# Kernel tuning notes

Hardware: AMD Instinct MI355X
Metric: run time of the kernel (lower is better)

The kernel has to match this reference:

```python
import jax, jax.numpy as jnp
import numpy as np

LOOKBACK = 1
LOOKAHEAD = 0
SEQ, BATCH, IN, HID = 1024, 16, 1024, 1024
K = LOOKBACK + 1 + LOOKAHEAD


def quick_gelu(x):
    return x * jax.nn.sigmoid(1.702 * x)


def setup_inputs() -> dict:
    key = jax.random.key(0)
    ks = jax.random.split(key, 5)
    scale = 1.0 / np.sqrt(IN * K)  # like torch Conv1d default init scale
    X = jax.random.normal(ks[0], (SEQ, BATCH, IN), dtype=jnp.float32)
    Wz = jax.random.normal(ks[1], (HID, IN, K), dtype=jnp.float32) * scale
    bz = jax.random.normal(ks[2], (HID,), dtype=jnp.float32) * scale
    Wf = jax.random.normal(ks[3], (HID, IN, K), dtype=jnp.float32) * scale
    bf = jax.random.normal(ks[4], (HID,), dtype=jnp.float32) * scale
    return {"X": X, "Wz": Wz, "bz": bz, "Wf": Wf, "bf": bf}


def _conv1d(x_pad, W, b):
    # x_pad: (B, Cin, T+K-1), W: (Cout, Cin, K) -> (B, Cout, T)
    y = jax.lax.conv_general_dilated(
        x_pad, W, window_strides=(1,), padding="VALID",
        dimension_numbers=("NCH", "OIH", "NCH"))
    return y + b[None, :, None]


def reference(X, Wz, bz, Wf, bf):
    # pad time dim: lookback zeros before, lookahead zeros after
    X_pad = jnp.pad(X, ((LOOKBACK, LOOKAHEAD), (0, 0), (0, 0)))
    X_pad = jnp.transpose(X_pad, (1, 2, 0))  # (B, Cin, T+K-1)
    Z = jnp.transpose(_conv1d(X_pad, Wz, bz), (2, 0, 1))  # (T, B, H)
    F = jnp.transpose(_conv1d(X_pad, Wf, bf), (2, 0, 1))  # (T, B, H)
    Z = quick_gelu(Z)
    F = jax.nn.sigmoid(F)

    def step(h, fz):
        f, z = fz
        h = f * z + (1.0 - f) * h
        return h, h

    h0 = jnp.zeros((BATCH, HID), dtype=X.dtype)
    _, H = jax.lax.scan(step, h0, (F, Z))  # H: (T, B, HID)
    return H, H[-1:, :, :]
```

## Files before the change

### kernel.cpp

```cpp
#include <hip/hip_runtime.h>
#include <stdint.h>

#define T_SEQ 1024
#define B_SZ  16
#define C_IN  1024
#define C_HID 1024
#define M_ROWS (T_SEQ * B_SZ)
#define N_COLS (2 * C_HID)
#define K_DIM  (2 * C_IN)

#define NCHUNK 16
#define CLEN   (T_SEQ / NCHUNK)
#define NBH    (B_SZ * C_HID)

typedef __attribute__((ext_vector_type(8))) short bf16x8;
typedef __attribute__((ext_vector_type(4))) float f32x4;
typedef unsigned short u16;

__device__ __forceinline__ u16 f2bf(float f) {
  union { float f; unsigned u; } v; v.f = f;
  unsigned r = v.u + 0x7fffu + ((v.u >> 16) & 1u);
  return (u16)(r >> 16);
}
__device__ __forceinline__ float bf2f(unsigned s) {
  union { unsigned u; float f; } v; v.u = s << 16;
  return v.f;
}

__device__ __forceinline__ void async_cp16(const u16* g, u16* l) {
  __builtin_amdgcn_global_load_lds(
      (const __attribute__((address_space(1))) unsigned*)(uintptr_t)g,
      (__attribute__((address_space(3))) unsigned*)(uintptr_t)l,
      16, 0, 0);
}

__global__ void k_convert_x(const float* __restrict__ X, u16* __restrict__ Xp) {
  int i = blockIdx.x * 256 + threadIdx.x;
  const int total4 = (M_ROWS + B_SZ) * C_IN / 4;
  if (i >= total4) return;
  int e = i << 2;
  const int PAD = B_SZ * C_IN;
  ushort4 o;
  if (e < PAD) {
    o.x = o.y = o.z = o.w = 0;
  } else {
    float4 v = *reinterpret_cast<const float4*>(X + (e - PAD));
    o.x = f2bf(v.x); o.y = f2bf(v.y); o.z = f2bf(v.z); o.w = f2bf(v.w);
  }
  *reinterpret_cast<ushort4*>(Xp + e) = o;
}

__global__ void k_repack_w(const float* __restrict__ Wz, const float* __restrict__ Wf,
                           u16* __restrict__ Wt) {
  int i = blockIdx.x * 256 + threadIdx.x;
  if (i >= 2 * 1024 * 1024) return;
  int g  = i >> 20;
  int hc = i & ((1 << 20) - 1);
  int h  = hc >> 10;
  int c  = hc & 1023;
  const float* W = g ? Wf : Wz;
  float2 w = *reinterpret_cast<const float2*>(W + ((size_t)(h << 10) + c) * 2);
  size_t n = ((size_t)h << 1) | (size_t)g;
  Wt[n * K_DIM + c]        = f2bf(w.x);
  Wt[n * K_DIM + 1024 + c] = f2bf(w.y);
}

__global__ __launch_bounds__(256, 2) void k_gemm(const u16* __restrict__ Xp,
                                                 const u16* __restrict__ Wt,
                                                 const float* __restrict__ bz,
                                                 const float* __restrict__ bfv,
                                                 u16* __restrict__ Cb) {
  __shared__ u16 sA[128 * 64];
  __shared__ u16 sB[128 * 64];
  const int tid  = threadIdx.x;
  const int wid  = tid >> 6;
  const int lane = tid & 63;
  const int m0 = blockIdx.x << 7;
  const int n0 = blockIdx.y << 7;
  const int wr = wid >> 1, wc = wid & 1;

  f32x4 acc[4][4] = {};

  const int srow = (wid << 5) + (lane >> 3);
  const int scol = (lane & 7) << 3;
  const int lr = lane & 15;
  const int lk = (lane >> 4) << 3;

  u16* lA = &sA[(wid << 5) << 6];
  u16* lB = &sB[(wid << 5) << 6];

  for (int kt = 0; kt < 32; ++kt) {
    const u16* gA = Xp + (size_t)(m0 + ((kt >= 16) ? B_SZ : 0) + srow) * C_IN
                       + ((kt & 15) << 6) + scol;
    const u16* gB = Wt + (size_t)(n0 + srow) * K_DIM + (kt << 6) + scol;
#pragma unroll
    for (int i = 0; i < 4; ++i) {
      async_cp16(gA + (size_t)(i << 3) * C_IN, lA + ((i << 3) << 6));
      async_cp16(gB + (size_t)(i << 3) * K_DIM, lB + ((i << 3) << 6));
    }
    __syncthreads();

#pragma unroll
    for (int ks = 0; ks < 2; ++ks) {
      bf16x8 a[4], b[4];
#pragma unroll
      for (int mi = 0; mi < 4; ++mi)
        a[mi] = *reinterpret_cast<const bf16x8*>(
            &sA[(((wr << 6) + (mi << 4) + lr) << 6) + (ks << 5) + lk]);
#pragma unroll
      for (int ni = 0; ni < 4; ++ni)
        b[ni] = *reinterpret_cast<const bf16x8*>(
            &sB[(((wc << 6) + (ni << 4) + lr) << 6) + (ks << 5) + lk]);
#pragma unroll
      for (int mi = 0; mi < 4; ++mi)
#pragma unroll
        for (int ni = 0; ni < 4; ++ni)
          acc[mi][ni] = __builtin_amdgcn_mfma_f32_16x16x32_bf16(
              a[mi], b[ni], acc[mi][ni], 0, 0, 0);
    }
    __syncthreads();
  }

  const int erow = (lane >> 4) << 2;
  const int ecol = lane & 15;
#pragma unroll
  for (int ni = 0; ni < 4; ++ni) {
    int col  = n0 + (wc << 6) + (ni << 4) + ecol;
    int hcol = col >> 1;
    bool isz = (col & 1) == 0;
    float bias = isz ? bz[hcol] : bfv[hcol];
    float kk   = isz ? 1.702f : 1.0f;
#pragma unroll
    for (int mi = 0; mi < 4; ++mi) {
      int row = m0 + (wr << 6) + (mi << 4) + erow;
#pragma unroll
      for (int r = 0; r < 4; ++r) {
        float v = acc[mi][ni][r] + bias;
        float s = 1.f / (1.f + __expf(-kk * v));
        float res = isz ? v * s : s;
        Cb[(size_t)(row + r) * N_COLS + col] = f2bf(res);
      }
    }
  }
}

__global__ __launch_bounds__(256) void k_scan1(const u16* __restrict__ Cb,
                                               float* __restrict__ Ap,
                                               float* __restrict__ Bp) {
  int i = blockIdx.x * 256 + threadIdx.x;
  int h = i & (C_HID - 1);
  int b = (i >> 10) & (B_SZ - 1);
  int c = i >> 14;
  const unsigned* Cu = (const unsigned*)Cb;
  size_t base = (size_t)b * C_HID + h + (size_t)c * CLEN * NBH;
  float hh = 0.f, P = 1.f;
#pragma unroll 16
  for (int t = 0; t < CLEN; ++t) {
    unsigned zf = Cu[base + (size_t)t * NBH];
    float z = bf2f(zf & 0xffffu);
    float f = bf2f(zf >> 16);
    hh += f * (z - hh);
    P  *= (1.f - f);
  }
  Ap[i] = hh;
  Bp[i] = P;
}

__global__ __launch_bounds__(256) void k_scan2(const float* __restrict__ Ap,
                                               const float* __restrict__ Bp,
                                               float* __restrict__ St) {
  int i = blockIdx.x * 256 + threadIdx.x;
  float hh = 0.f;
#pragma unroll
  for (int c = 0; c < NCHUNK; ++c) {
    St[c * NBH + i] = hh;
    hh = Ap[c * NBH + i] + Bp[c * NBH + i] * hh;
  }
}

__global__ __launch_bounds__(256) void k_scan3(const u16* __restrict__ Cb,
                                               const float* __restrict__ St,
                                               float* __restrict__ out) {
  int i = blockIdx.x * 256 + threadIdx.x;
  int bh = i & (NBH - 1);
  int c = i >> 14;
  const unsigned* Cu = (const unsigned*)Cb;
  size_t base = (size_t)bh + (size_t)c * CLEN * NBH;
  float hh = St[i];
#pragma unroll 16
  for (int t = 0; t < CLEN; ++t) {
    unsigned zf = Cu[base + (size_t)t * NBH];
    float z = bf2f(zf & 0xffffu);
    float f = bf2f(zf >> 16);
    hh += f * (z - hh);
    out[base + (size_t)t * NBH] = hh;
  }
  if (c == NCHUNK - 1)
    out[(size_t)M_ROWS * C_HID + bh] = hh;
}

extern "C" void kernel_launch(void* const* d_in, const int* in_sizes, int n_in,
                              void* d_out, int out_size, void* d_ws, size_t ws_size,
                              hipStream_t stream) {
  const float* X   = (const float*)d_in[0];
  const float* Wz  = (const float*)d_in[1];
  const float* bz  = (const float*)d_in[2];
  const float* Wf  = (const float*)d_in[3];
  const float* bf_ = (const float*)d_in[4];
  float* out = (float*)d_out;

  u16* Xp = (u16*)d_ws;
  u16* Wt = Xp + (size_t)(M_ROWS + B_SZ) * C_IN;
  u16* Cb = Wt + (size_t)N_COLS * K_DIM;
  float* Ap = (float*)Xp;
  float* Bp = Ap + NCHUNK * NBH;
  float* St = Bp + NCHUNK * NBH;

  hipLaunchKernelGGL(k_convert_x, dim3(16400), dim3(256), 0, stream, X, Xp);
  hipLaunchKernelGGL(k_repack_w, dim3(8192), dim3(256), 0, stream, Wz, Wf, Wt);
  hipLaunchKernelGGL(k_gemm, dim3(M_ROWS / 128, N_COLS / 128), dim3(256), 0, stream,
                     Xp, Wt, bz, bf_, Cb);
  hipLaunchKernelGGL(k_scan1, dim3(NCHUNK * NBH / 256), dim3(256), 0, stream,
                     Cb, Ap, Bp);
  hipLaunchKernelGGL(k_scan2, dim3(NBH / 256), dim3(256), 0, stream, Ap, Bp, St);
  hipLaunchKernelGGL(k_scan3, dim3(NCHUNK * NBH / 256), dim3(256), 0, stream,
                     Cb, St, out);
}
```

Before: 328.7 us.

## Rewrite GEMM as 256x256 tile, 8-wave, double-buffered pipelined kernel with swizzled LDS

Replaces the 128x128 single-buffered GEMM with a 256x256-tile kernel using 8 waves and double-buffered LDS. Global-to-LDS async loads are issued in quarter stages interleaved with MFMA phases, paced by explicit vmcnt waits, barriers and setprio. An XOR swizzle on the LDS layout is meant to avoid bank conflicts, and block indices are remapped for better L2 locality. The aim is to hide load latency and raise MFMA utilisation, at the cost of higher register pressure (32 accumulators per lane) and fragile hand-written wait counts.

```diff
diff --git a/kernel.cpp b/kernel.cpp
--- a/kernel.cpp
+++ b/kernel.cpp
@@ -16,6 +16,8 @@
 typedef __attribute__((ext_vector_type(8))) short bf16x8;
 typedef __attribute__((ext_vector_type(4))) float f32x4;
 typedef unsigned short u16;
+
+#define MFMA __builtin_amdgcn_mfma_f32_16x16x32_bf16
 
 __device__ __forceinline__ u16 f2bf(float f) {
   union { float f; unsigned u; } v; v.f = f;
@@ -65,60 +67,142 @@
   Wt[n * K_DIM + 1024 + c] = f2bf(w.y);
 }
 
-__global__ __launch_bounds__(256, 2) void k_gemm(const u16* __restrict__ Xp,
-                                                 const u16* __restrict__ Wt,
-                                                 const float* __restrict__ bz,
-                                                 const float* __restrict__ bfv,
-                                                 u16* __restrict__ Cb) {
-  __shared__ u16 sA[128 * 64];
-  __shared__ u16 sB[128 * 64];
+__global__ __launch_bounds__(512, 2) void k_gemm8(const u16* __restrict__ Xp,
+                                                  const u16* __restrict__ Wt,
+                                                  const float* __restrict__ bz,
+                                                  const float* __restrict__ bfv,
+                                                  u16* __restrict__ Cb) {
+  __shared__ u16 lds[2][2][2][8192];
   const int tid  = threadIdx.x;
+  const int lane = tid & 63;
   const int wid  = tid >> 6;
-  const int lane = tid & 63;
-  const int m0 = blockIdx.x << 7;
-  const int n0 = blockIdx.y << 7;
-  const int wr = wid >> 1, wc = wid & 1;
-
-  f32x4 acc[4][4] = {};
-
-  const int srow = (wid << 5) + (lane >> 3);
-  const int scol = (lane & 7) << 3;
+  const int wr = wid >> 2;
+  const int wc = wid & 3;
   const int lr = lane & 15;
-  const int lk = (lane >> 4) << 3;
-
-  u16* lA = &sA[(wid << 5) << 6];
-  u16* lB = &sB[(wid << 5) << 6];
-
-  for (int kt = 0; kt < 32; ++kt) {
-    const u16* gA = Xp + (size_t)(m0 + ((kt >= 16) ? B_SZ : 0) + srow) * C_IN
-                       + ((kt & 15) << 6) + scol;
-    const u16* gB = Wt + (size_t)(n0 + srow) * K_DIM + (kt << 6) + scol;
-#pragma unroll
-    for (int i = 0; i < 4; ++i) {
-      async_cp16(gA + (size_t)(i << 3) * C_IN, lA + ((i << 3) << 6));
-      async_cp16(gB + (size_t)(i << 3) * K_DIM, lB + ((i << 3) << 6));
+
+  int wg = (blockIdx.x & 7) * 64 + (blockIdx.x >> 3);
+  const int m0 = (wg >> 3) << 8;
+  const int n0 = (wg & 7) << 8;
+
+  const int p    = tid << 4;
+  const int q    = p ^ (((p >> 7) & 7) << 4);
+  const int grow = q >> 7;
+  const int gcol = (q & 127) >> 1;
+  const int ldsw = (tid >> 6) << 9;
+
+  const int rbase = lr << 6;
+  int co[2];
+#pragma unroll
+  for (int ks = 0; ks < 2; ++ks)
+    co[ks] = ((((ks << 6) | ((lane >> 4) << 4)) ^ ((lr & 7) << 4)) >> 1);
+
+  auto stage = [&](int j) {
+    int kt = j >> 2, part = j & 3, buf = kt & 1;
+    if (part >= 2) {
+      int h = part - 2;
+      const u16* g = Xp + (size_t)(m0 + (h << 7) + grow + ((kt >= 16) ? B_SZ : 0)) * C_IN
+                        + ((kt & 15) << 6) + gcol;
+      u16* l = &lds[buf][0][h][ldsw];
+      async_cp16(g, l);
+      async_cp16(g + (size_t)64 * C_IN, l + 4096);
+    } else {
+      const u16* g = Wt + (size_t)(n0 + (part << 7) + grow) * K_DIM + (kt << 6) + gcol;
+      u16* l = &lds[buf][1][part][ldsw];
+      async_cp16(g, l);
+      async_cp16(g + (size_t)64 * K_DIM, l + 4096);
     }
-    __syncthreads();
-
-#pragma unroll
-    for (int ks = 0; ks < 2; ++ks) {
-      bf16x8 a[4], b[4];
-#pragma unroll
-      for (int mi = 0; mi < 4; ++mi)
-        a[mi] = *reinterpret_cast<const bf16x8*>(
-            &sA[(((wr << 6) + (mi << 4) + lr) << 6) + (ks << 5) + lk]);
-#pragma unroll
-      for (int ni = 0; ni < 4; ++ni)
-        b[ni] = *reinterpret_cast<const bf16x8*>(
-            &sB[(((wc << 6) + (ni << 4) + lr) << 6) + (ks << 5) + lk]);
-#pragma unroll
-      for (int mi = 0; mi < 4; ++mi)
-#pragma unroll
-        for (int ni = 0; ni < 4; ++ni)
-          acc[mi][ni] = __builtin_amdgcn_mfma_f32_16x16x32_bf16(
-              a[mi], b[ni], acc[mi][ni], 0, 0, 0);
-    }
-    __syncthreads();
+  };
+
+  f32x4 acc[8][4] = {};
+  bf16x8 a[4][2], b0[2][2], b1[2][2];
+
+  for (int j = 0; j < 7; ++j) stage(j);
+  asm volatile("s_waitcnt vmcnt(6)" ::: "memory");
+  __builtin_amdgcn_s_barrier();
+
+#pragma unroll 2
+  for (int t = 0; t < 32; ++t) {
+    const int buf = t & 1;
+    const u16* pA = &lds[buf][0][wr][0];
+    const u16* pB = &lds[buf][1][wc >> 1][(wc & 1) << 12];
+    const int jb = 4 * t + 7;
+
+#pragma unroll
+    for (int mi = 0; mi < 4; ++mi)
+#pragma unroll
+      for (int ks = 0; ks < 2; ++ks)
+        a[mi][ks] = *(const bf16x8*)(pA + (mi << 10) + rbase + co[ks]);
+#pragma unroll
+    for (int ni = 0; ni < 2; ++ni)
+#pragma unroll
+      for (int ks = 0; ks < 2; ++ks)
+        b0[ni][ks] = *(const bf16x8*)(pB + (ni << 10) + rbase + co[ks]);
+    if (jb < 128) stage(jb);
+    __builtin_amdgcn_s_barrier();
+    asm volatile("s_waitcnt lgkmcnt(0)" ::: "memory");
+    __builtin_amdgcn_s_setprio(1);
+#pragma unroll
+    for (int mi = 0; mi < 4; ++mi)
+#pragma unroll
+      for (int ni = 0; ni < 2; ++ni)
+#pragma unroll
+        for (int ks = 0; ks < 2; ++ks)
+          acc[mi][ni] = MFMA(a[mi][ks], b0[ni][ks], acc[mi][ni], 0, 0, 0);
+    __builtin_amdgcn_s_setprio(0);
+    __builtin_amdgcn_s_barrier();
+
+#pragma unroll
+    for (int ni = 0; ni < 2; ++ni)
+#pragma unroll
+      for (int ks = 0; ks < 2; ++ks)
+        b1[ni][ks] = *(const bf16x8*)(pB + ((2 + ni) << 10) + rbase + co[ks]);
+    if (jb + 1 < 128) stage(jb + 1);
+    __builtin_amdgcn_s_barrier();
+    asm volatile("s_waitcnt lgkmcnt(0)" ::: "memory");
+    __builtin_amdgcn_s_setprio(1);
+#pragma unroll
+    for (int mi = 0; mi < 4; ++mi)
+#pragma unroll
+      for (int ni = 0; ni < 2; ++ni)
+#pragma unroll
+        for (int ks = 0; ks < 2; ++ks)
+          acc[mi][2 + ni] = MFMA(a[mi][ks], b1[ni][ks], acc[mi][2 + ni], 0, 0, 0);
+    __builtin_amdgcn_s_setprio(0);
+    __builtin_amdgcn_s_barrier();
+
+#pragma unroll
+    for (int mi = 0; mi < 4; ++mi)
+#pragma unroll
+      for (int ks = 0; ks < 2; ++ks)
+        a[mi][ks] = *(const bf16x8*)(pA + ((4 + mi) << 10) + rbase + co[ks]);
+    if (jb + 2 < 128) stage(jb + 2);
+    __builtin_amdgcn_s_barrier();
+    asm volatile("s_waitcnt lgkmcnt(0)" ::: "memory");
+    __builtin_amdgcn_s_setprio(1);
+#pragma unroll
+    for (int mi = 0; mi < 4; ++mi)
+#pragma unroll
+      for (int ni = 0; ni < 2; ++ni)
+#pragma unroll
+        for (int ks = 0; ks < 2; ++ks)
+          acc[4 + mi][2 + ni] = MFMA(a[mi][ks], b1[ni][ks], acc[4 + mi][2 + ni], 0, 0, 0);
+    __builtin_amdgcn_s_setprio(0);
+    __builtin_amdgcn_s_barrier();
+
+    if (jb + 3 < 128) stage(jb + 3);
+    if (t < 30) asm volatile("s_waitcnt vmcnt(6)" ::: "memory");
+    else        asm volatile("s_waitcnt vmcnt(0)" ::: "memory");
+    __builtin_amdgcn_s_barrier();
+    __builtin_amdgcn_s_setprio(1);
+#pragma unroll
+    for (int mi = 0; mi < 4; ++mi)
+#pragma unroll
+      for (int ni = 0; ni < 2; ++ni)
+#pragma unroll
+        for (int ks = 0; ks < 2; ++ks)
+          acc[4 + mi][ni] = MFMA(a[mi][ks], b0[ni][ks], acc[4 + mi][ni], 0, 0, 0);
+    __builtin_amdgcn_s_setprio(0);
+    __builtin_amdgcn_s_barrier();
   }
 
   const int erow = (lane >> 4) << 2;
@@ -131,8 +215,8 @@
     float bias = isz ? bz[hcol] : bfv[hcol];
     float kk   = isz ? 1.702f : 1.0f;
 #pragma unroll
-    for (int mi = 0; mi < 4; ++mi) {
-      int row = m0 + (wr << 6) + (mi << 4) + erow;
+    for (int mi = 0; mi < 8; ++mi) {
+      int row = m0 + (wr << 7) + (mi << 4) + erow;
 #pragma unroll
       for (int r = 0; r < 4; ++r) {
         float v = acc[mi][ni][r] + bias;
@@ -218,8 +302,8 @@
 
   hipLaunchKernelGGL(k_convert_x, dim3(16400), dim3(256), 0, stream, X, Xp);
   hipLaunchKernelGGL(k_repack_w, dim3(8192), dim3(256), 0, stream, Wz, Wf, Wt);
-  hipLaunchKernelGGL(k_gemm, dim3(M_ROWS / 128, N_COLS / 128), dim3(256), 0, stream,
-                     Xp, Wt, bz, bf_, Cb);
+  hipLaunchKernelGGL(k_gemm8, dim3((M_ROWS / 256) * (N_COLS / 256)), dim3(512), 0,
+                     stream, Xp, Wt, bz, bf_, Cb);
   hipLaunchKernelGGL(k_scan1, dim3(NCHUNK * NBH / 256), dim3(256), 0, stream,
                      Cb, Ap, Bp);
   hipLaunchKernelGGL(k_scan2, dim3(NBH / 256), dim3(256), 0, stream, Ap, Bp, St);
```

New measurement: 308.1 us. -6.2%, faster.
